# Optimization experiments

Measured on AMD Instinct MI355X. Metric: run time of the kernel, lower is better.

Reference implementation:

```python
import jax, jax.numpy as jnp
import numpy as np

D_MODEL = 256
OUT_DIM = 256
D_STATE = 16
D_CONV = 4
EXPAND = 2
D_INNER = EXPAND * D_MODEL  # 512
DT_RANK = (D_MODEL + 15) // 16  # 16
B_SZ, L = 2, 4096


def setup_inputs() -> dict:
    key = jax.random.key(0)
    ks = jax.random.split(key, 12)
    s = lambda *sh: 0.02
    inp = {}
    inp['x'] = jax.random.normal(ks[0], (B_SZ, L, D_MODEL), jnp.float32)
    inp['ln_w'] = jnp.ones((D_MODEL,), jnp.float32)
    inp['ln_b'] = jnp.zeros((D_MODEL,), jnp.float32)
    inp['in_proj_w'] = jax.random.normal(ks[1], (2 * D_INNER, D_MODEL), jnp.float32) * 0.02
    inp['conv_w'] = jax.random.normal(ks[2], (D_INNER, 1, D_CONV), jnp.float32) * 0.2
    inp['conv_b'] = jnp.zeros((D_INNER,), jnp.float32)
    inp['x_proj_w'] = jax.random.normal(ks[3], (DT_RANK + 2 * D_STATE, D_INNER), jnp.float32) * 0.02
    inp['dt_proj_w'] = jax.random.normal(ks[4], (D_INNER, DT_RANK), jnp.float32) * 0.05
    inp['dt_proj_b'] = jax.random.uniform(ks[5], (D_INNER,), jnp.float32, -4.0, -2.0)  # small dt after softplus
    inp['A_log'] = jnp.log(jnp.broadcast_to(jnp.arange(1, D_STATE + 1, dtype=jnp.float32), (D_INNER, D_STATE)))
    inp['Dskip'] = jnp.ones((D_INNER,), jnp.float32)
    inp['out_proj_w'] = jax.random.normal(ks[6], (D_MODEL, D_INNER), jnp.float32) * 0.02
    inp['proj_w'] = jax.random.normal(ks[7], (OUT_DIM, D_MODEL), jnp.float32) * 0.02
    inp['proj_b'] = jnp.zeros((OUT_DIM,), jnp.float32)
    inp['skip_scale'] = jnp.ones((1,), jnp.float32)
    return inp


def _layernorm(x, w, b, eps=1e-5):
    mu = jnp.mean(x, axis=-1, keepdims=True)
    var = jnp.var(x, axis=-1, keepdims=True)
    return (x - mu) * jax.lax.rsqrt(var + eps) * w + b


def _selective_scan(u, delta, A, Bm, Cm, Dskip):
    # u, delta: (B,L,d); A: (d,n); Bm, Cm: (B,L,n)
    dA = jnp.exp(delta[..., None] * A)                       # (B,L,d,n)
    dBu = (delta * u)[..., None] * Bm[:, :, None, :]          # (B,L,d,n)
    h0 = jnp.zeros((u.shape[0], A.shape[0], A.shape[1]), u.dtype)

    def step(h, inp):
        dA_t, dBu_t, C_t = inp
        h = dA_t * h + dBu_t                                  # (B,d,n)
        y = jnp.einsum('bdn,bn->bd', h, C_t)
        return h, y

    xs = (dA.transpose(1, 0, 2, 3), dBu.transpose(1, 0, 2, 3), Cm.transpose(1, 0, 2))
    _, ys = jax.lax.scan(step, h0, xs)                        # (L,B,d)
    return ys.transpose(1, 0, 2) + u * Dskip


def _mamba(xn, in_proj_w, conv_w, conv_b, x_proj_w, dt_proj_w, dt_proj_b, A_log, Dskip, out_proj_w):
    # xn: (B,L,d_model)
    xz = jnp.einsum('bld,ed->ble', xn, in_proj_w)             # (B,L,2*d_inner)
    xi, z = jnp.split(xz, 2, axis=-1)
    # depthwise causal conv over L
    xc = jax.lax.conv_general_dilated(
        xi.transpose(0, 2, 1), conv_w, window_strides=(1,),
        padding=[(D_CONV - 1, 0)], feature_group_count=D_INNER,
        dimension_numbers=('NCH', 'OIH', 'NCH'))
    xc = (xc + conv_b[None, :, None]).transpose(0, 2, 1)       # (B,L,d_inner)
    xc = jax.nn.silu(xc)
    dbc = jnp.einsum('bld,ed->ble', xc, x_proj_w)             # (B,L,dt_rank+2n)
    dt, Bm, Cm = jnp.split(dbc, [DT_RANK, DT_RANK + D_STATE], axis=-1)
    delta = jax.nn.softplus(jnp.einsum('blr,dr->bld', dt, dt_proj_w) + dt_proj_b)
    A = -jnp.exp(A_log)                                       # (d_inner, n)
    y = _selective_scan(xc, delta, A, Bm, Cm, Dskip)
    y = y * jax.nn.silu(z)
    return jnp.einsum('ble,de->bld', y, out_proj_w)


def reference(x, ln_w, ln_b, in_proj_w, conv_w, conv_b, x_proj_w, dt_proj_w, dt_proj_b,
              A_log, Dskip, out_proj_w, proj_w, proj_b, skip_scale):
    x_norm = _layernorm(x, ln_w, ln_b)
    x_mamba = _mamba(x_norm, in_proj_w, conv_w, conv_b, x_proj_w, dt_proj_w, dt_proj_b,
                     A_log, Dskip, out_proj_w) + skip_scale * x
    x_mamba = _layernorm(x_mamba, ln_w, ln_b)
    return jnp.einsum('bld,od->blo', x_mamba, proj_w) + proj_b
```

## Files before the change

kernel.cpp:

```cpp
#include <hip/hip_runtime.h>
#include <hip/hip_bf16.h>

#define B_SZ   2
#define LSEQ   4096
#define NCH    256
#define CL     16

typedef __attribute__((ext_vector_type(8))) short short8;
typedef __attribute__((ext_vector_type(4))) float f32x4;

__device__ __forceinline__ unsigned short f2bf(float f) {
  union { float f; unsigned u; } x; x.f = f;
  unsigned r = x.u + 0x7fffu + ((x.u >> 16) & 1u);
  return (unsigned short)(r >> 16);
}

__device__ __forceinline__ void gload_lds16(const unsigned short* g, unsigned short* l) {
  __builtin_amdgcn_global_load_lds(
      (const __attribute__((address_space(1))) unsigned int*)g,
      (__attribute__((address_space(3))) unsigned int*)l, 16, 0, 0);
}

__global__ __launch_bounds__(256) void f2bf4_kernel(
    const float* __restrict__ in, unsigned short* __restrict__ out)
{
  int i = (blockIdx.x * 256 + threadIdx.x) * 4;
  float4 v = *reinterpret_cast<const float4*>(in + i);
  ushort4 o;
  o.x = f2bf(v.x); o.y = f2bf(v.y); o.z = f2bf(v.z); o.w = f2bf(v.w);
  *reinterpret_cast<ushort4*>(out + i) = o;
}

__global__ __launch_bounds__(256) void ln_bf_kernel(
    const float* __restrict__ in, const float* __restrict__ w,
    const float* __restrict__ b, unsigned short* __restrict__ out)
{
  int wv = threadIdx.x >> 6, lane = threadIdx.x & 63;
  size_t row = (size_t)blockIdx.x * 4 + wv;
  float4 v = reinterpret_cast<const float4*>(in)[row * 64 + lane];
  float s  = v.x + v.y + v.z + v.w;
  float sq = v.x*v.x + v.y*v.y + v.z*v.z + v.w*v.w;
  #pragma unroll
  for (int off = 32; off; off >>= 1) {
    s  += __shfl_xor(s,  off);
    sq += __shfl_xor(sq, off);
  }
  float mu  = s * (1.f/256.f);
  float var = sq * (1.f/256.f) - mu*mu;
  float rs  = rsqrtf(var + 1e-5f);
  float4 wv4 = reinterpret_cast<const float4*>(w)[lane];
  float4 bv4 = reinterpret_cast<const float4*>(b)[lane];
  ushort4 o;
  o.x = f2bf((v.x-mu)*rs*wv4.x + bv4.x);
  o.y = f2bf((v.y-mu)*rs*wv4.y + bv4.y);
  o.z = f2bf((v.z-mu)*rs*wv4.z + bv4.z);
  o.w = f2bf((v.w-mu)*rs*wv4.w + bv4.w);
  reinterpret_cast<ushort4*>(out)[row * 64 + lane] = o;
}

enum { EPI_NONE = 0, EPI_SKIPX = 1, EPI_BIAS = 2 };

template<int BM, int BN, int EPI>
__global__ __launch_bounds__(256) void gemm_mfma(
    const unsigned short* __restrict__ A, const unsigned short* __restrict__ W,
    float* __restrict__ C, int M, int N, int K,
    const float* __restrict__ X, const float* __restrict__ sscale,
    const float* __restrict__ bias)
{
  constexpr int BK = 32;
  constexpr int WM = BM / 2, WN = BN / 2;
  constexpr int AM = WM / 16, BF = WN / 16;
  constexpr int AI = BM / 64, BI = BN / 64;
  __shared__ __align__(16) unsigned short As[2][BM * BK];
  __shared__ __align__(16) unsigned short Ws[2][BN * BK];
  const int tid = threadIdx.x, lane = tid & 63, wid = tid >> 6;
  const int wr = wid >> 1, wc = wid & 1;
  const int bm = blockIdx.x * BM, bn = blockIdx.y * BN;
  const int srow = lane >> 2;
  const int skoff = (lane & 3) * 8;

  f32x4 acc[AM][BF] = {};

  auto stage = [&](int buf, int kt) {
    #pragma unroll
    for (int i = 0; i < AI; i++) {
      int rowg = (wid * AI + i) * 16;
      gload_lds16(A + (size_t)(bm + rowg + srow) * K + kt + skoff,
                  &As[buf][rowg * BK]);
    }
    #pragma unroll
    for (int i = 0; i < BI; i++) {
      int rowg = (wid * BI + i) * 16;
      gload_lds16(W + (size_t)(bn + rowg + srow) * K + kt + skoff,
                  &Ws[buf][rowg * BK]);
    }
  };

  stage(0, 0);
  __syncthreads();
  const int nt = K / BK;
  int cur = 0;
  for (int t = 0; t < nt; t++) {
    if (t + 1 < nt) stage(cur ^ 1, (t + 1) * BK);
    short8 af[AM], bfr[BF];
    #pragma unroll
    for (int i = 0; i < AM; i++)
      af[i] = *reinterpret_cast<const short8*>(
          &As[cur][(wr * WM + i * 16 + (lane & 15)) * BK + (lane >> 4) * 8]);
    #pragma unroll
    for (int j = 0; j < BF; j++)
      bfr[j] = *reinterpret_cast<const short8*>(
          &Ws[cur][(wc * WN + j * 16 + (lane & 15)) * BK + (lane >> 4) * 8]);
    #pragma unroll
    for (int i = 0; i < AM; i++)
      #pragma unroll
      for (int j = 0; j < BF; j++)
        acc[i][j] = __builtin_amdgcn_mfma_f32_16x16x32_bf16(af[i], bfr[j], acc[i][j], 0, 0, 0);
    __syncthreads();
    cur ^= 1;
  }

  float sv = 0.f;
  if constexpr (EPI == EPI_SKIPX) sv = sscale[0];

  #pragma unroll
  for (int i = 0; i < AM; i++) {
    #pragma unroll
    for (int j = 0; j < BF; j++) {
      int row0 = bm + wr * WM + i * 16 + ((lane >> 4) << 2);
      int col  = bn + wc * WN + j * 16 + (lane & 15);
      #pragma unroll
      for (int r = 0; r < 4; r++) {
        float v = acc[i][j][r];
        size_t off = (size_t)(row0 + r) * N + col;
        if constexpr (EPI == EPI_SKIPX) v += sv * X[off];
        if constexpr (EPI == EPI_BIAS)  v += bias[col];
        C[off] = v;
      }
    }
  }
}

__global__ __launch_bounds__(256) void gemm_mfma48(
    const unsigned short* __restrict__ A, const unsigned short* __restrict__ W,
    float* __restrict__ C, int K)
{
  __shared__ __align__(16) unsigned short As[2][64 * 32];
  __shared__ __align__(16) unsigned short Ws[2][48 * 32];
  const int tid = threadIdx.x, lane = tid & 63, wid = tid >> 6;
  const int bm = blockIdx.x * 64;
  const int srow = lane >> 2, skoff = (lane & 3) * 8;

  f32x4 acc[3] = {};

  auto stage = [&](int buf, int kt) {
    int rowg = wid * 16;
    gload_lds16(A + (size_t)(bm + rowg + srow) * K + kt + skoff, &As[buf][rowg * 32]);
    if (wid < 3)
      gload_lds16(W + (size_t)(rowg + srow) * K + kt + skoff, &Ws[buf][rowg * 32]);
  };

  stage(0, 0);
  __syncthreads();
  const int nt = K / 32;
  int cur = 0;
  for (int t = 0; t < nt; t++) {
    if (t + 1 < nt) stage(cur ^ 1, (t + 1) * 32);
    short8 af = *reinterpret_cast<const short8*>(
        &As[cur][(wid * 16 + (lane & 15)) * 32 + (lane >> 4) * 8]);
    #pragma unroll
    for (int j = 0; j < 3; j++) {
      short8 bfr = *reinterpret_cast<const short8*>(
          &Ws[cur][(j * 16 + (lane & 15)) * 32 + (lane >> 4) * 8]);
      acc[j] = __builtin_amdgcn_mfma_f32_16x16x32_bf16(af, bfr, acc[j], 0, 0, 0);
    }
    __syncthreads();
    cur ^= 1;
  }
  int row0 = bm + wid * 16 + ((lane >> 4) << 2);
  #pragma unroll
  for (int j = 0; j < 3; j++) {
    int col = j * 16 + (lane & 15);
    #pragma unroll
    for (int r = 0; r < 4; r++)
      C[(size_t)(row0 + r) * 48 + col] = acc[j][r];
  }
}

__global__ __launch_bounds__(256) void conv_silu_kernel(
    const float* __restrict__ xz, const float* __restrict__ cw,
    const float* __restrict__ cb, float* __restrict__ xc,
    unsigned short* __restrict__ xc_bf)
{
  int idx = blockIdx.x * 256 + threadIdx.x;
  int d4 = (idx & 127) << 2;
  int bt = idx >> 7;
  int t  = bt & (LSEQ - 1);
  int b  = bt >> 12;
  float a0 = cb[d4], a1 = cb[d4+1], a2 = cb[d4+2], a3 = cb[d4+3];
  float4 w0 = *reinterpret_cast<const float4*>(&cw[(d4+0)*4]);
  float4 w1 = *reinterpret_cast<const float4*>(&cw[(d4+1)*4]);
  float4 w2 = *reinterpret_cast<const float4*>(&cw[(d4+2)*4]);
  float4 w3 = *reinterpret_cast<const float4*>(&cw[(d4+3)*4]);
  const float* wp0 = (const float*)&w0;
  const float* wp1 = (const float*)&w1;
  const float* wp2 = (const float*)&w2;
  const float* wp3 = (const float*)&w3;
  #pragma unroll
  for (int j = 0; j < 4; j++) {
    int tt = t - 3 + j;
    if (tt >= 0) {
      float4 xv = *reinterpret_cast<const float4*>(&xz[((size_t)b*LSEQ + tt)*1024 + d4]);
      a0 += wp0[j]*xv.x; a1 += wp1[j]*xv.y; a2 += wp2[j]*xv.z; a3 += wp3[j]*xv.w;
    }
  }
  float4 o;
  o.x = a0 / (1.f + __expf(-a0));
  o.y = a1 / (1.f + __expf(-a1));
  o.z = a2 / (1.f + __expf(-a2));
  o.w = a3 / (1.f + __expf(-a3));
  size_t ro = ((size_t)b*LSEQ + t)*512 + d4;
  *reinterpret_cast<float4*>(&xc[ro]) = o;
  ushort4 ob;
  ob.x = f2bf(o.x); ob.y = f2bf(o.y); ob.z = f2bf(o.z); ob.w = f2bf(o.w);
  *reinterpret_cast<ushort4*>(&xc_bf[ro]) = ob;
}

__global__ __launch_bounds__(256) void dtproj_kernel(
    const float* __restrict__ dbc, const float* __restrict__ dpw,
    const float* __restrict__ dpb, float* __restrict__ delta)
{
  int tid = threadIdx.x;
  size_t row = (size_t)blockIdx.x * 2 + (tid >> 7);
  int d0 = (tid & 127) << 2;
  const float4* dt = reinterpret_cast<const float4*>(dbc + row * 48);
  float4 t0 = dt[0], t1 = dt[1], t2 = dt[2], t3 = dt[3];
  float4 out;
  float* op = (float*)&out;
  #pragma unroll
  for (int dd = 0; dd < 4; dd++) {
    int d = d0 + dd;
    const float4* wr = reinterpret_cast<const float4*>(&dpw[d*16]);
    float4 w0 = wr[0], w1 = wr[1], w2 = wr[2], w3 = wr[3];
    float acc = dpb[d];
    acc += t0.x*w0.x + t0.y*w0.y + t0.z*w0.z + t0.w*w0.w;
    acc += t1.x*w1.x + t1.y*w1.y + t1.z*w1.z + t1.w*w1.w;
    acc += t2.x*w2.x + t2.y*w2.y + t2.z*w2.z + t2.w*w2.w;
    acc += t3.x*w3.x + t3.y*w3.y + t3.z*w3.z + t3.w*w3.w;
    op[dd] = fmaxf(acc, 0.f) + log1pf(__expf(-fabsf(acc)));
  }
  *reinterpret_cast<float4*>(&delta[row * 512 + d0]) = out;
}

__global__ __launch_bounds__(256) void scanA_kernel(
    const float* __restrict__ delta, const float* __restrict__ xc,
    const float* __restrict__ dbc, const float* __restrict__ A_log,
    float* __restrict__ hloc, float* __restrict__ Ssum)
{
  int g = blockIdx.x * 256 + threadIdx.x;
  int nh = g & 1;
  int d  = (g >> 1) & 511;
  int c  = (g >> 10) & (NCH - 1);
  int b  = g >> 18;
  const float4* Ap = reinterpret_cast<const float4*>(A_log + d*16 + nh*8);
  float4 A0 = Ap[0], A1 = Ap[1];
  float Ar[8] = {-__expf(A0.x), -__expf(A0.y), -__expf(A0.z), -__expf(A0.w),
                 -__expf(A1.x), -__expf(A1.y), -__expf(A1.z), -__expf(A1.w)};
  float h[8] = {};
  float S = 0.f;
  size_t tbase = (size_t)b * LSEQ + (size_t)c * CL;
  for (int t = 0; t < CL; t++) {
    size_t r = tbase + t;
    float dl = delta[r*512 + d];
    float u  = xc[r*512 + d];
    float du = dl * u;
    S += dl;
    const float4* Bp = reinterpret_cast<const float4*>(dbc + r*48 + 16 + nh*8);
    float4 B0 = Bp[0], B1 = Bp[1];
    float Bv[8] = {B0.x,B0.y,B0.z,B0.w, B1.x,B1.y,B1.z,B1.w};
    #pragma unroll
    for (int n = 0; n < 8; n++)
      h[n] = __expf(dl * Ar[n]) * h[n] + du * Bv[n];
  }
  size_t o = (((size_t)c * B_SZ + b) * 512 + d) * 16 + nh*8;
  float4 h0 = {h[0],h[1],h[2],h[3]}, h1 = {h[4],h[5],h[6],h[7]};
  *reinterpret_cast<float4*>(&hloc[o])   = h0;
  *reinterpret_cast<float4*>(&hloc[o+4]) = h1;
  if (nh == 0) Ssum[((size_t)c * B_SZ + b) * 512 + d] = S;
}

__global__ __launch_bounds__(256) void scanmid2_kernel(
    const float* __restrict__ hloc, const float* __restrict__ Ssum,
    const float* __restrict__ A_log, float* __restrict__ henter)
{
  int g = blockIdx.x * 256 + threadIdx.x;
  int n = g & 15, d = (g >> 4) & 511, b = g >> 13;
  float Ar = -__expf(A_log[d*16 + n]);
  float h = 0.f;
  #pragma unroll 4
  for (int c = 0; c < NCH; c++) {
    size_t idx = ((size_t)c * B_SZ + b) * 512 + d;
    henter[idx*16 + n] = h;
    h = __expf(Ssum[idx] * Ar) * h + hloc[idx*16 + n];
  }
}

__global__ __launch_bounds__(256) void scanB_kernel(
    const float* __restrict__ delta, const float* __restrict__ xc,
    const float* __restrict__ dbc, const float* __restrict__ A_log,
    const float* __restrict__ henter, const float* __restrict__ Dskip,
    const float* __restrict__ xz, unsigned short* __restrict__ y_bf)
{
  int g = blockIdx.x * 256 + threadIdx.x;
  int nh = g & 1;
  int d  = (g >> 1) & 511;
  int c  = (g >> 10) & (NCH - 1);
  int b  = g >> 18;
  const float4* Ap = reinterpret_cast<const float4*>(A_log + d*16 + nh*8);
  float4 A0 = Ap[0], A1 = Ap[1];
  float Ar[8] = {-__expf(A0.x), -__expf(A0.y), -__expf(A0.z), -__expf(A0.w),
                 -__expf(A1.x), -__expf(A1.y), -__expf(A1.z), -__expf(A1.w)};
  size_t o = (((size_t)c * B_SZ + b) * 512 + d) * 16 + nh*8;
  float4 h0 = *reinterpret_cast<const float4*>(&henter[o]);
  float4 h1 = *reinterpret_cast<const float4*>(&henter[o+4]);
  float h[8] = {h0.x,h0.y,h0.z,h0.w, h1.x,h1.y,h1.z,h1.w};
  float Dsk = Dskip[d];
  size_t tbase = (size_t)b * LSEQ + (size_t)c * CL;
  for (int t = 0; t < CL; t++) {
    size_t r = tbase + t;
    float dl = delta[r*512 + d];
    float u  = xc[r*512 + d];
    float du = dl * u;
    const float4* Bp = reinterpret_cast<const float4*>(dbc + r*48 + 16 + nh*8);
    const float4* Cp = reinterpret_cast<const float4*>(dbc + r*48 + 32 + nh*8);
    float4 B0 = Bp[0], B1 = Bp[1];
    float4 C0 = Cp[0], C1 = Cp[1];
    float Bv[8] = {B0.x,B0.y,B0.z,B0.w, B1.x,B1.y,B1.z,B1.w};
    float Cv[8] = {C0.x,C0.y,C0.z,C0.w, C1.x,C1.y,C1.z,C1.w};
    float yp = 0.f;
    #pragma unroll
    for (int n = 0; n < 8; n++) {
      h[n] = __expf(dl * Ar[n]) * h[n] + du * Bv[n];
      yp += h[n] * Cv[n];
    }
    float y = yp + __shfl_xor(yp, 1);
    if (nh == 0) {
      y += u * Dsk;
      float z = xz[r*1024 + 512 + d];
      float sig = 1.f / (1.f + __expf(-z));
      y_bf[r*512 + d] = f2bf(y * z * sig);
    }
  }
}

extern "C" void kernel_launch(void* const* d_in, const int* in_sizes, int n_in,
                              void* d_out, int out_size, void* d_ws, size_t ws_size,
                              hipStream_t stream)
{
  const float* x      = (const float*)d_in[0];
  const float* ln_w   = (const float*)d_in[1];
  const float* ln_b   = (const float*)d_in[2];
  const float* inW    = (const float*)d_in[3];
  const float* convW  = (const float*)d_in[4];
  const float* convB  = (const float*)d_in[5];
  const float* xprojW = (const float*)d_in[6];
  const float* dtW    = (const float*)d_in[7];
  const float* dtB    = (const float*)d_in[8];
  const float* A_log  = (const float*)d_in[9];
  const float* Dskip  = (const float*)d_in[10];
  const float* outW   = (const float*)d_in[11];
  const float* projW  = (const float*)d_in[12];
  const float* projB  = (const float*)d_in[13];
  const float* skip   = (const float*)d_in[14];
  float* out = (float*)d_out;

  const size_t BL = (size_t)B_SZ * LSEQ;
  char* p = (char*)d_ws;
  unsigned short* xn_bf = (unsigned short*)p;  p += BL*256*2;
  float* xz     = (float*)p;                   p += BL*1024*4;
  float* xc     = (float*)p;                   p += BL*512*4;
  float* dbc    = (float*)p;                   p += BL*48*4;
  float* delta  = (float*)p;                   p += BL*512*4;
  float* hloc   = (float*)p;                   p += (size_t)NCH*B_SZ*512*16*4;
  float* henter = (float*)p;                   p += (size_t)NCH*B_SZ*512*16*4;
  float* Ssum   = (float*)p;                   p += (size_t)NCH*B_SZ*512*4;
  unsigned short* y_bf = (unsigned short*)p;   p += BL*512*2;
  unsigned short* inW_bf  = (unsigned short*)p; p += 1024*256*2;
  unsigned short* outW_bf = (unsigned short*)p; p += 256*512*2;
  unsigned short* projW_bf= (unsigned short*)p; p += 256*256*2;
  unsigned short* xprojW_bf=(unsigned short*)p; p += 48*512*2;
  unsigned short* xc_bf = (unsigned short*)henter;
  float* xm = hloc;
  unsigned short* xn2_bf = xn_bf;

  f2bf4_kernel<<<1024*256/1024, 256, 0, stream>>>(inW,  inW_bf);
  f2bf4_kernel<<<256*512/1024, 256, 0, stream>>>(outW, outW_bf);
  f2bf4_kernel<<<256*256/1024, 256, 0, stream>>>(projW, projW_bf);
  f2bf4_kernel<<<48*512/1024, 256, 0, stream>>>(xprojW, xprojW_bf);

  ln_bf_kernel<<<BL/4, 256, 0, stream>>>(x, ln_w, ln_b, xn_bf);

  gemm_mfma<128,128,EPI_NONE><<<dim3(BL/128, 1024/128), 256, 0, stream>>>(
      xn_bf, inW_bf, xz, (int)BL, 1024, 256, nullptr, nullptr, nullptr);

  conv_silu_kernel<<<(B_SZ*LSEQ*128)/256, 256, 0, stream>>>(xz, convW, convB, xc, xc_bf);

  gemm_mfma48<<<BL/64, 256, 0, stream>>>(xc_bf, xprojW_bf, dbc, 512);

  dtproj_kernel<<<BL/2, 256, 0, stream>>>(dbc, dtW, dtB, delta);

  scanA_kernel<<<(B_SZ*NCH*512*2)/256, 256, 0, stream>>>(delta, xc, dbc, A_log, hloc, Ssum);
  scanmid2_kernel<<<B_SZ*512*16/256, 256, 0, stream>>>(hloc, Ssum, A_log, henter);
  scanB_kernel<<<(B_SZ*NCH*512*2)/256, 256, 0, stream>>>(delta, xc, dbc, A_log, henter, Dskip, xz, y_bf);

  gemm_mfma<64,64,EPI_SKIPX><<<dim3(BL/64, 256/64), 256, 0, stream>>>(
      y_bf, outW_bf, xm, (int)BL, 256, 512, x, skip, nullptr);

  ln_bf_kernel<<<BL/4, 256, 0, stream>>>(xm, ln_w, ln_b, xn2_bf);

  gemm_mfma<64,64,EPI_BIAS><<<dim3(BL/64, 256/64), 256, 0, stream>>>(
      xn2_bf, projW_bf, out, (int)BL, 256, 256, nullptr, nullptr, projB);
}
```

Measured before the change: 263.3 us.

## Fuse dt projection and softplus into scan kernels, read bf16 conv output

Removes the standalone dtproj kernel and its fp32 delta buffer. Both scan passes now recompute delta per timestep from the 16 dt values in dbc and per-channel weights held in registers. The fp32 xc buffer is dropped, and the scans read the bf16 xc copy that the x_proj GEMM already uses. This cuts a kernel launch and several large fp32 global reads and writes in exchange for extra FMAs and transcendentals computed twice (in scanA and scanB), plus reduced precision of u in the scan.

```diff
diff --git a/kernel.cpp b/kernel.cpp
--- a/kernel.cpp
+++ b/kernel.cpp
@@ -13,6 +13,10 @@
   union { float f; unsigned u; } x; x.f = f;
   unsigned r = x.u + 0x7fffu + ((x.u >> 16) & 1u);
   return (unsigned short)(r >> 16);
+}
+__device__ __forceinline__ float bf2f(unsigned short u) {
+  union { unsigned u; float f; } x; x.u = (unsigned)u << 16;
+  return x.f;
 }
 
 __device__ __forceinline__ void gload_lds16(const unsigned short* g, unsigned short* l) {
@@ -189,8 +193,7 @@
 
 __global__ __launch_bounds__(256) void conv_silu_kernel(
     const float* __restrict__ xz, const float* __restrict__ cw,
-    const float* __restrict__ cb, float* __restrict__ xc,
-    unsigned short* __restrict__ xc_bf)
+    const float* __restrict__ cb, unsigned short* __restrict__ xc_bf)
 {
   int idx = blockIdx.x * 256 + threadIdx.x;
   int d4 = (idx & 127) << 2;
@@ -214,47 +217,33 @@
       a0 += wp0[j]*xv.x; a1 += wp1[j]*xv.y; a2 += wp2[j]*xv.z; a3 += wp3[j]*xv.w;
     }
   }
-  float4 o;
-  o.x = a0 / (1.f + __expf(-a0));
-  o.y = a1 / (1.f + __expf(-a1));
-  o.z = a2 / (1.f + __expf(-a2));
-  o.w = a3 / (1.f + __expf(-a3));
-  size_t ro = ((size_t)b*LSEQ + t)*512 + d4;
-  *reinterpret_cast<float4*>(&xc[ro]) = o;
   ushort4 ob;
-  ob.x = f2bf(o.x); ob.y = f2bf(o.y); ob.z = f2bf(o.z); ob.w = f2bf(o.w);
-  *reinterpret_cast<ushort4*>(&xc_bf[ro]) = ob;
-}
-
-__global__ __launch_bounds__(256) void dtproj_kernel(
-    const float* __restrict__ dbc, const float* __restrict__ dpw,
-    const float* __restrict__ dpb, float* __restrict__ delta)
-{
-  int tid = threadIdx.x;
-  size_t row = (size_t)blockIdx.x * 2 + (tid >> 7);
-  int d0 = (tid & 127) << 2;
-  const float4* dt = reinterpret_cast<const float4*>(dbc + row * 48);
+  ob.x = f2bf(a0 / (1.f + __expf(-a0)));
+  ob.y = f2bf(a1 / (1.f + __expf(-a1)));
+  ob.z = f2bf(a2 / (1.f + __expf(-a2)));
+  ob.w = f2bf(a3 / (1.f + __expf(-a3)));
+  *reinterpret_cast<ushort4*>(&xc_bf[((size_t)b*LSEQ + t)*512 + d4]) = ob;
+}
+
+__device__ __forceinline__ float delta_of(const float* __restrict__ dbc_row,
+                                          const float4* __restrict__ wp,
+                                          float bias)
+{
+  const float4* dt = reinterpret_cast<const float4*>(dbc_row);
   float4 t0 = dt[0], t1 = dt[1], t2 = dt[2], t3 = dt[3];
-  float4 out;
-  float* op = (float*)&out;
-  #pragma unroll
-  for (int dd = 0; dd < 4; dd++) {
-    int d = d0 + dd;
-    const float4* wr = reinterpret_cast<const float4*>(&dpw[d*16]);
-    float4 w0 = wr[0], w1 = wr[1], w2 = wr[2], w3 = wr[3];
-    float acc = dpb[d];
-    acc += t0.x*w0.x + t0.y*w0.y + t0.z*w0.z + t0.w*w0.w;
-    acc += t1.x*w1.x + t1.y*w1.y + t1.z*w1.z + t1.w*w1.w;
-    acc += t2.x*w2.x + t2.y*w2.y + t2.z*w2.z + t2.w*w2.w;
-    acc += t3.x*w3.x + t3.y*w3.y + t3.z*w3.z + t3.w*w3.w;
-    op[dd] = fmaxf(acc, 0.f) + log1pf(__expf(-fabsf(acc)));
-  }
-  *reinterpret_cast<float4*>(&delta[row * 512 + d0]) = out;
+  float4 w0 = wp[0], w1 = wp[1], w2 = wp[2], w3 = wp[3];
+  float acc = bias;
+  acc += t0.x*w0.x + t0.y*w0.y + t0.z*w0.z + t0.w*w0.w;
+  acc += t1.x*w1.x + t1.y*w1.y + t1.z*w1.z + t1.w*w1.w;
+  acc += t2.x*w2.x + t2.y*w2.y + t2.z*w2.z + t2.w*w2.w;
+  acc += t3.x*w3.x + t3.y*w3.y + t3.z*w3.z + t3.w*w3.w;
+  return fmaxf(acc, 0.f) + log1pf(__expf(-fabsf(acc)));
 }
 
 __global__ __launch_bounds__(256) void scanA_kernel(
-    const float* __restrict__ delta, const float* __restrict__ xc,
-    const float* __restrict__ dbc, const float* __restrict__ A_log,
+    const float* __restrict__ dbc, const unsigned short* __restrict__ xc_bf,
+    const float* __restrict__ A_log,
+    const float* __restrict__ dpw, const float* __restrict__ dpb,
     float* __restrict__ hloc, float* __restrict__ Ssum)
 {
   int g = blockIdx.x * 256 + threadIdx.x;
@@ -266,13 +255,16 @@
   float4 A0 = Ap[0], A1 = Ap[1];
   float Ar[8] = {-__expf(A0.x), -__expf(A0.y), -__expf(A0.z), -__expf(A0.w),
                  -__expf(A1.x), -__expf(A1.y), -__expf(A1.z), -__expf(A1.w)};
+  const float4* wp4 = reinterpret_cast<const float4*>(dpw + d*16);
+  float4 dw[4] = {wp4[0], wp4[1], wp4[2], wp4[3]};
+  float dbias = dpb[d];
   float h[8] = {};
   float S = 0.f;
   size_t tbase = (size_t)b * LSEQ + (size_t)c * CL;
   for (int t = 0; t < CL; t++) {
     size_t r = tbase + t;
-    float dl = delta[r*512 + d];
-    float u  = xc[r*512 + d];
+    float dl = delta_of(dbc + r*48, dw, dbias);
+    float u  = bf2f(xc_bf[r*512 + d]);
     float du = dl * u;
     S += dl;
     const float4* Bp = reinterpret_cast<const float4*>(dbc + r*48 + 16 + nh*8);
@@ -306,8 +298,9 @@
 }
 
 __global__ __launch_bounds__(256) void scanB_kernel(
-    const float* __restrict__ delta, const float* __restrict__ xc,
-    const float* __restrict__ dbc, const float* __restrict__ A_log,
+    const float* __restrict__ dbc, const unsigned short* __restrict__ xc_bf,
+    const float* __restrict__ A_log,
+    const float* __restrict__ dpw, const float* __restrict__ dpb,
     const float* __restrict__ henter, const float* __restrict__ Dskip,
     const float* __restrict__ xz, unsigned short* __restrict__ y_bf)
 {
@@ -320,6 +313,9 @@
   float4 A0 = Ap[0], A1 = Ap[1];
   float Ar[8] = {-__expf(A0.x), -__expf(A0.y), -__expf(A0.z), -__expf(A0.w),
                  -__expf(A1.x), -__expf(A1.y), -__expf(A1.z), -__expf(A1.w)};
+  const float4* wp4 = reinterpret_cast<const float4*>(dpw + d*16);
+  float4 dw[4] = {wp4[0], wp4[1], wp4[2], wp4[3]};
+  float dbias = dpb[d];
   size_t o = (((size_t)c * B_SZ + b) * 512 + d) * 16 + nh*8;
   float4 h0 = *reinterpret_cast<const float4*>(&henter[o]);
   float4 h1 = *reinterpret_cast<const float4*>(&henter[o+4]);
@@ -328,8 +324,8 @@
   size_t tbase = (size_t)b * LSEQ + (size_t)c * CL;
   for (int t = 0; t < CL; t++) {
     size_t r = tbase + t;
-    float dl = delta[r*512 + d];
-    float u  = xc[r*512 + d];
+    float dl = delta_of(dbc + r*48, dw, dbias);
+    float u  = bf2f(xc_bf[r*512 + d]);
     float du = dl * u;
     const float4* Bp = reinterpret_cast<const float4*>(dbc + r*48 + 16 + nh*8);
     const float4* Cp = reinterpret_cast<const float4*>(dbc + r*48 + 32 + nh*8);
@@ -378,9 +374,8 @@
   char* p = (char*)d_ws;
   unsigned short* xn_bf = (unsigned short*)p;  p += BL*256*2;
   float* xz     = (float*)p;                   p += BL*1024*4;
-  float* xc     = (float*)p;                   p += BL*512*4;
+  unsigned short* xc_bf = (unsigned short*)p;  p += BL*512*2;
   float* dbc    = (float*)p;                   p += BL*48*4;
-  float* delta  = (float*)p;                   p += BL*512*4;
   float* hloc   = (float*)p;                   p += (size_t)NCH*B_SZ*512*16*4;
   float* henter = (float*)p;                   p += (size_t)NCH*B_SZ*512*16*4;
   float* Ssum   = (float*)p;                   p += (size_t)NCH*B_SZ*512*4;
@@ -389,7 +384,6 @@
   unsigned short* outW_bf = (unsigned short*)p; p += 256*512*2;
   unsigned short* projW_bf= (unsigned short*)p; p += 256*256*2;
   unsigned short* xprojW_bf=(unsigned short*)p; p += 48*512*2;
-  unsigned short* xc_bf = (unsigned short*)henter;
   float* xm = hloc;
   unsigned short* xn2_bf = xn_bf;
 
@@ -403,15 +397,15 @@
   gemm_mfma<128,128,EPI_NONE><<<dim3(BL/128, 1024/128), 256, 0, stream>>>(
       xn_bf, inW_bf, xz, (int)BL, 1024, 256, nullptr, nullptr, nullptr);
 
-  conv_silu_kernel<<<(B_SZ*LSEQ*128)/256, 256, 0, stream>>>(xz, convW, convB, xc, xc_bf);
+  conv_silu_kernel<<<(B_SZ*LSEQ*128)/256, 256, 0, stream>>>(xz, convW, convB, xc_bf);
 
   gemm_mfma48<<<BL/64, 256, 0, stream>>>(xc_bf, xprojW_bf, dbc, 512);
 
-  dtproj_kernel<<<BL/2, 256, 0, stream>>>(dbc, dtW, dtB, delta);
-
-  scanA_kernel<<<(B_SZ*NCH*512*2)/256, 256, 0, stream>>>(delta, xc, dbc, A_log, hloc, Ssum);
+  scanA_kernel<<<(B_SZ*NCH*512*2)/256, 256, 0, stream>>>(
+      dbc, xc_bf, A_log, dtW, dtB, hloc, Ssum);
   scanmid2_kernel<<<B_SZ*512*16/256, 256, 0, stream>>>(hloc, Ssum, A_log, henter);
-  scanB_kernel<<<(B_SZ*NCH*512*2)/256, 256, 0, stream>>>(delta, xc, dbc, A_log, henter, Dskip, xz, y_bf);
+  scanB_kernel<<<(B_SZ*NCH*512*2)/256, 256, 0, stream>>>(
+      dbc, xc_bf, A_log, dtW, dtB, henter, Dskip, xz, y_bf);
 
   gemm_mfma<64,64,EPI_SKIPX><<<dim3(BL/64, 256/64), 256, 0, stream>>>(
       y_bf, outW_bf, xm, (int)BL, 256, 512, x, skip, nullptr);
```

New measurement: 292.4 us. 1.11x slower.
